# Performance work log

Hardware: AMD Instinct MI355X
Metric: run time of the kernel (lower is better)

The kernel has to match this reference:

```python
import jax, jax.numpy as jnp
import numpy as np

HIDDEN = 1024
EMBED = 1024
SEQ = 512
BATCH = 64


def setup_inputs() -> dict:
    key = jax.random.key(0)
    k1, k2, k3 = jax.random.split(key, 3)
    factor = 1.0 / np.sqrt(HIDDEN)
    embeds = jax.random.normal(k1, (SEQ, BATCH, EMBED), dtype=jnp.float32)
    w = jax.random.uniform(k2, (HIDDEN + EMBED, 4 * HIDDEN), dtype=jnp.float32,
                           minval=-factor, maxval=factor)
    b = jax.random.uniform(k3, (4 * HIDDEN,), dtype=jnp.float32,
                           minval=-factor, maxval=factor)
    # forget-gate bias += 1 (gate order is g, i, f, o)
    b = b.at[2 * HIDDEN:3 * HIDDEN].add(1.0)
    return {"embeds": embeds, "w": w, "b": b}


def reference(embeds, w, b):
    T, B, E = embeds.shape
    H = w.shape[1] // 4

    def step(carry, x_t):
        h, c = carry
        data = jnp.concatenate([h, x_t], axis=-1)          # [B, H+E]
        big = data @ w + b                                  # [B, 4H]
        g, i, f, o = jnp.split(big, 4, axis=1)
        g = jnp.tanh(g)
        i = jax.nn.sigmoid(i)
        f = jax.nn.sigmoid(f)
        o = jax.nn.sigmoid(o)
        c_new = g * i + c * f
        h_new = jnp.tanh(c_new) * o
        return (h_new, c_new), h_new

    h0 = jnp.zeros((B, H), dtype=embeds.dtype)
    c0 = jnp.zeros((B, H), dtype=embeds.dtype)
    _, out = jax.lax.scan(step, (h0, c0), embeds)           # out: [T, B, H]
    return out
```

## Files before the change

kernel.cpp:

```cpp
#include <hip/hip_runtime.h>
#include <stdint.h>


#define TSTEPS 512
#define NBATCH 64
#define NHID   1024
#define NWG2   64
#define FLAGSTRIDE 32
#define AGENT  __HIP_MEMORY_SCOPE_AGENT

typedef __attribute__((ext_vector_type(8))) short bf16x8;
typedef __attribute__((ext_vector_type(4))) float f32x4;
typedef __attribute__((ext_vector_type(4))) int   i32x4;
typedef __attribute__((ext_vector_type(4))) float fl4;

__device__ __forceinline__ uint16_t f2bf(float f){
  uint32_t u = __float_as_uint(f);
  u += 0x7fffu + ((u >> 16) & 1u);
  return (uint16_t)(u >> 16);
}
__device__ __forceinline__ float bf2f(uint16_t b){
  return __uint_as_float(((uint32_t)b) << 16);
}
__device__ __forceinline__ float sigm(float x){ return 1.0f/(1.0f + __expf(-x)); }
__device__ __forceinline__ float tanhfast(float x){ return 1.0f - 2.0f/(__expf(2.0f*x) + 1.0f); }
__device__ __forceinline__ bf16x8 as_bf(i32x4 v){
  union { i32x4 i; bf16x8 b; } u; u.i = v; return u.b;
}

__global__ void k0a_cvt(const float* __restrict__ in, uint16_t* __restrict__ outp, int n8){
  int stride = gridDim.x * blockDim.x;
  for (int i = blockIdx.x * blockDim.x + threadIdx.x; i < n8; i += stride){
    const fl4* p = (const fl4*)(in + (size_t)i * 8);
    fl4 v0 = p[0], v1 = p[1];
    union { uint16_t u[8]; i32x4 v; } r;
    r.u[0]=f2bf(v0.x); r.u[1]=f2bf(v0.y); r.u[2]=f2bf(v0.z); r.u[3]=f2bf(v0.w);
    r.u[4]=f2bf(v1.x); r.u[5]=f2bf(v1.y); r.u[6]=f2bf(v1.z); r.u[7]=f2bf(v1.w);
    *(i32x4*)(outp + (size_t)i * 8) = r.v;
  }
}

__global__ void k0b_trans(const float* __restrict__ w, uint16_t* __restrict__ wT){
  __shared__ float tile[64 * 65];
  int k0 = blockIdx.x * 64;
  int n0 = blockIdx.y * 64;
  int tid = threadIdx.x;
  int r  = tid >> 2;
  int cq = (tid & 3) * 16;
#pragma unroll
  for (int i = 0; i < 4; ++i){
    fl4 v = *(const fl4*)(w + (size_t)(k0 + r) * 4096 + n0 + cq + i * 4);
    tile[r*65 + cq + i*4 + 0] = v.x;
    tile[r*65 + cq + i*4 + 1] = v.y;
    tile[r*65 + cq + i*4 + 2] = v.z;
    tile[r*65 + cq + i*4 + 3] = v.w;
  }
  __syncthreads();
  union { uint16_t u[8]; i32x4 v; } a, b;
#pragma unroll
  for (int i = 0; i < 8; ++i) a.u[i] = f2bf(tile[(cq + i) * 65 + r]);
#pragma unroll
  for (int i = 0; i < 8; ++i) b.u[i] = f2bf(tile[(cq + 8 + i) * 65 + r]);
  *(i32x4*)(wT + (size_t)(n0 + r) * 2048 + k0 + cq)     = a.v;
  *(i32x4*)(wT + (size_t)(n0 + r) * 2048 + k0 + cq + 8) = b.v;
}

__launch_bounds__(256, 2)
__global__ void k1_xw(const uint16_t* __restrict__ ebf, const uint16_t* __restrict__ wT,
                      const float* __restrict__ bias, uint16_t* __restrict__ xw){
  __shared__ char sm[32768];
  char* As = sm;
  char* Bs = sm + 16384;
  int bid = blockIdx.x;
  int nt = bid & 31, mt = bid >> 5;
  int m0 = mt * 128, n0 = nt * 128;
  int tid = threadIdx.x;
  int lane = tid & 63, wid = tid >> 6;
  int wr = wid >> 1, wc = wid & 1;

  f32x4 zero = {0.f, 0.f, 0.f, 0.f};
  f32x4 acc[4][4];
#pragma unroll
  for (int mi = 0; mi < 4; ++mi)
#pragma unroll
    for (int ni = 0; ni < 4; ++ni) acc[mi][ni] = zero;

  for (int kt = 0; kt < 16; ++kt){
    __syncthreads();
#pragma unroll
    for (int i = 0; i < 4; ++i){
      int L = i * 256 + tid;
      int row = L >> 3, c = L & 7;
      i32x4 va = *(const i32x4*)(ebf + (size_t)(m0 + row) * 1024 + kt * 64 + c * 8);
      *(i32x4*)(As + row * 128 + ((c ^ (row & 7)) * 16)) = va;
      i32x4 vb = *(const i32x4*)(wT + (size_t)(n0 + row) * 2048 + 1024 + kt * 64 + c * 8);
      *(i32x4*)(Bs + row * 128 + ((c ^ (row & 7)) * 16)) = vb;
    }
    __syncthreads();
#pragma unroll
    for (int kk = 0; kk < 2; ++kk){
      bf16x8 a[4], b[4];
      int ci = kk * 4 + (lane >> 4);
#pragma unroll
      for (int mi = 0; mi < 4; ++mi){
        int rl = wr * 64 + mi * 16 + (lane & 15);
        a[mi] = *(const bf16x8*)(As + rl * 128 + ((ci ^ (rl & 7)) * 16));
      }
#pragma unroll
      for (int ni = 0; ni < 4; ++ni){
        int sl = wc * 64 + ni * 16 + (lane & 15);
        b[ni] = *(const bf16x8*)(Bs + sl * 128 + ((ci ^ (sl & 7)) * 16));
      }
#pragma unroll
      for (int mi = 0; mi < 4; ++mi)
#pragma unroll
        for (int ni = 0; ni < 4; ++ni)
          acc[mi][ni] = __builtin_amdgcn_mfma_f32_16x16x32_bf16(a[mi], b[ni], acc[mi][ni], 0, 0, 0);
    }
  }
  float bcol[4];
#pragma unroll
  for (int ni = 0; ni < 4; ++ni) bcol[ni] = bias[n0 + wc * 64 + ni * 16 + (lane & 15)];
#pragma unroll
  for (int mi = 0; mi < 4; ++mi)
#pragma unroll
    for (int ni = 0; ni < 4; ++ni)
#pragma unroll
      for (int jj = 0; jj < 4; ++jj){
        int rg = m0 + wr * 64 + mi * 16 + (lane >> 4) * 4 + jj;
        int cg = n0 + wc * 64 + ni * 16 + (lane & 15);
        xw[(size_t)rg * 4096 + cg] = f2bf(acc[mi][ni][jj] + bcol[ni]);
      }
}

#define LDA(k, OFF) asm volatile("global_load_dwordx4 %0, %1, off offset:" #OFF \
                                 : "=v"(ap[k]) : "v"(aB) : "memory")
#define WAITV(N) do { asm volatile("s_waitcnt vmcnt(" #N ")" ::: "memory"); \
                      __builtin_amdgcn_sched_barrier(0); } while(0)
#define GBLK(K0) \
  _Pragma("unroll") \
  for (int kc = K0; kc < K0 + 8; ++kc){ \
    bf16x8 a = as_bf(ap[kc]); \
    _Pragma("unroll") \
    for (int g = 0; g < 4; ++g){ \
      bf16x8 b = *(const bf16x8*)(WP + ((kc * 4 + g) << 10) + (lane << 4)); \
      acc[g] = __builtin_amdgcn_mfma_f32_16x16x32_bf16(a, b, acc[g], 0, 0, 0); \
    } \
  }

__launch_bounds__(256, 1)
__global__ void k2_rec(const uint16_t* __restrict__ xw, const uint16_t* __restrict__ wT,
                       uint16_t* __restrict__ hbuf, int* __restrict__ flags,
                       float* __restrict__ outp){
  extern __shared__ char sm[];
  char* WP = sm;

  int tid  = threadIdx.x;
  int lane = tid & 63;
  int wid  = tid >> 6;
  int wg = blockIdx.x;
  int j0 = wg * 16;

#pragma unroll
  for (int i = 0; i < 32; ++i){
    int L = i * 256 + tid;
    int kc = L >> 8;
    int g  = (L >> 6) & 3;
    int l6 = L & 63;
    int q  = (l6 >> 4) & 3;
    int rr = l6 & 15;
    i32x4 v = *(const i32x4*)(wT + (size_t)(g * 1024 + j0 + rr) * 2048 + kc * 32 + q * 8);
    *(i32x4*)(WP + (size_t)L * 16) = v;
  }
  __syncthreads();

  const int r0 = wid * 16;
  const int q  = lane >> 4;
  const int rr = lane & 15;

  float creg[4] = {0.f, 0.f, 0.f, 0.f};

  uint16_t xc[4][4];
  {
    const uint16_t* xp = xw + (size_t)0 * (64 * 4096) + j0 + rr;
#pragma unroll
    for (int g = 0; g < 4; ++g)
#pragma unroll
      for (int p = 0; p < 4; ++p)
        xc[g][p] = xp[(size_t)(r0 + q * 4 + p) * 4096 + g * 1024];
  }

  for (int t = 0; t < TSTEPS; ++t){
    if (t > 0){
      if (tid < 64){
        while (true){
          int v = __hip_atomic_load(&flags[tid * FLAGSTRIDE], __ATOMIC_RELAXED, AGENT);
          if (__all(v >= t)) break;
          __builtin_amdgcn_s_sleep(1);
        }
      }
      __syncthreads();
    }

    const uint16_t* hsrc = hbuf + (size_t)t * (NBATCH * NHID);
    const uint16_t* aB = hsrc + (size_t)(r0 + rr) * 1024 + q * 8;
    i32x4 ap[32];
    LDA(0,0);     LDA(1,64);    LDA(2,128);   LDA(3,192);
    LDA(4,256);   LDA(5,320);   LDA(6,384);   LDA(7,448);
    LDA(8,512);   LDA(9,576);   LDA(10,640);  LDA(11,704);
    LDA(12,768);  LDA(13,832);  LDA(14,896);  LDA(15,960);
    LDA(16,1024); LDA(17,1088); LDA(18,1152); LDA(19,1216);
    LDA(20,1280); LDA(21,1344); LDA(22,1408); LDA(23,1472);
    LDA(24,1536); LDA(25,1600); LDA(26,1664); LDA(27,1728);
    LDA(28,1792); LDA(29,1856); LDA(30,1920); LDA(31,1984);

    uint16_t xn[4][4];
    {
      int tn = (t < TSTEPS - 1) ? t + 1 : t;
      const uint16_t* xp = xw + (size_t)tn * (64 * 4096) + j0 + rr;
#pragma unroll
      for (int g = 0; g < 4; ++g)
#pragma unroll
        for (int p = 0; p < 4; ++p)
          xn[g][p] = xp[(size_t)(r0 + q * 4 + p) * 4096 + g * 1024];
    }

    f32x4 acc[4];
#pragma unroll
    for (int g = 0; g < 4; ++g) acc[g] = (f32x4){0.f, 0.f, 0.f, 0.f};

    WAITV(40); GBLK(0);
    WAITV(32); GBLK(8);
    WAITV(24); GBLK(16);
    WAITV(16); GBLK(24);

    uint16_t* hdst = hbuf + (size_t)(t + 1) * (NBATCH * NHID);
    float*    odst = outp + (size_t)t * (NBATCH * NHID);
    float hv[4];
#pragma unroll
    for (int p = 0; p < 4; ++p){
      float G = acc[0][p] + bf2f(xc[0][p]);
      float I = acc[1][p] + bf2f(xc[1][p]);
      float F = acc[2][p] + bf2f(xc[2][p]);
      float O = acc[3][p] + bf2f(xc[3][p]);
      G = tanhfast(G); I = sigm(I); F = sigm(F); O = sigm(O);
      float c = G * I + creg[p] * F;
      creg[p] = c;
      float h = tanhfast(c) * O;
      hv[p] = h;
      __hip_atomic_store(hbuf + (size_t)(t + 1) * (NBATCH * NHID)
                              + (size_t)(r0 + q * 4 + p) * 1024 + j0 + rr,
                         f2bf(h), __ATOMIC_RELAXED, AGENT);
    }
    (void)hdst;

#pragma unroll
    for (int g = 0; g < 4; ++g)
#pragma unroll
      for (int p = 0; p < 4; ++p)
        xc[g][p] = xn[g][p];

    asm volatile("s_waitcnt vmcnt(0)" ::: "memory");
    __syncthreads();
    if (tid == 0)
      __hip_atomic_store(&flags[wg * FLAGSTRIDE], t + 1, __ATOMIC_RELAXED, AGENT);

#pragma unroll
    for (int p = 0; p < 4; ++p)
      odst[(size_t)(r0 + q * 4 + p) * 1024 + j0 + rr] = hv[p];
  }
}

extern "C" void kernel_launch(void* const* d_in, const int* in_sizes, int n_in,
                              void* d_out, int out_size, void* d_ws, size_t ws_size,
                              hipStream_t stream){
  const float* embeds = (const float*)d_in[0];
  const float* w      = (const float*)d_in[1];
  const float* bias   = (const float*)d_in[2];
  float* outp = (float*)d_out;
  char* ws = (char*)d_ws;

  const size_t o_ebf = 0;
  const size_t o_wT  = o_ebf + (size_t)32768 * 1024 * 2;
  const size_t o_xw  = o_wT  + (size_t)4096 * 2048 * 2;
  const size_t o_hb  = o_xw  + (size_t)32768 * 4096 * 2;
  const size_t o_fl  = o_hb  + (size_t)513 * 64 * 1024 * 2;

  uint16_t* ebf  = (uint16_t*)(ws + o_ebf);
  uint16_t* wT   = (uint16_t*)(ws + o_wT);
  uint16_t* xw   = (uint16_t*)(ws + o_xw);
  uint16_t* hbuf = (uint16_t*)(ws + o_hb);
  int*      flags= (int*)(ws + o_fl);

  hipMemsetAsync(ws + o_hb, 0, (size_t)64 * 1024 * 2, stream);
  hipMemsetAsync(ws + o_fl, 0, NWG2 * FLAGSTRIDE * sizeof(int), stream);

  k0a_cvt<<<2048, 256, 0, stream>>>(embeds, ebf, (512 * 64 * 1024) / 8);
  k0b_trans<<<dim3(32, 64), 256, 0, stream>>>(w, wT);
  k1_xw<<<8192, 256, 0, stream>>>(ebf, wT, bias, xw);

  (void)hipFuncSetAttribute((const void*)k2_rec,
                            hipFuncAttributeMaxDynamicSharedMemorySize, 131072);
  k2_rec<<<NWG2, 256, 131072, stream>>>(xw, wT, hbuf, flags, outp);
}
```

Before: 4.525 ms.

## Split recurrent tile 2x2 across waves with per-wave flags and LDS gate exchange

Each workgroup's four waves now each compute a 32-row by 2-gate sub-tile instead of 16 rows by all four gates. Results are exchanged through an extra LDS buffer so every thread gets all four gates for its elements. The step barrier is replaced by per-wave flags: each wave publishes its own flag, and each wave polls only the flags of the row half it reads. This removes the single-wave poll plus block barrier on the critical path and halves LDS weight reads per MFMA. It adds an LDS exchange and a __syncthreads per step, doubles the A-register footprint, and raises dynamic LDS above 128KB.

```diff
diff --git a/kernel.cpp b/kernel.cpp
--- a/kernel.cpp
+++ b/kernel.cpp
@@ -133,19 +133,21 @@
       }
 }
 
-#define LDA(k, OFF) asm volatile("global_load_dwordx4 %0, %1, off offset:" #OFF \
-                                 : "=v"(ap[k]) : "v"(aB) : "memory")
+#define LDA(k, BASE, OFF) asm volatile("global_load_dwordx4 %0, %1, off offset:" #OFF \
+                                 : "=v"(ap[k]) : "v"(BASE) : "memory")
 #define WAITV(N) do { asm volatile("s_waitcnt vmcnt(" #N ")" ::: "memory"); \
                       __builtin_amdgcn_sched_barrier(0); } while(0)
-#define GBLK(K0) \
+#define GBLK(NB) \
   _Pragma("unroll") \
-  for (int kc = K0; kc < K0 + 8; ++kc){ \
-    bf16x8 a = as_bf(ap[kc]); \
-    _Pragma("unroll") \
-    for (int g = 0; g < 4; ++g){ \
-      bf16x8 b = *(const bf16x8*)(WP + ((kc * 4 + g) << 10) + (lane << 4)); \
-      acc[g] = __builtin_amdgcn_mfma_f32_16x16x32_bf16(a, b, acc[g], 0, 0, 0); \
-    } \
+  for (int kc = (NB) * 4; kc < (NB) * 4 + 4; ++kc){ \
+    bf16x8 b0 = *(const bf16x8*)(WP + ((kc * 4 + 0) << 10) + chB + (lane << 4)); \
+    bf16x8 b1 = *(const bf16x8*)(WP + ((kc * 4 + 1) << 10) + chB + (lane << 4)); \
+    bf16x8 a0 = as_bf(ap[kc * 2 + 0]); \
+    bf16x8 a1 = as_bf(ap[kc * 2 + 1]); \
+    acc00 = __builtin_amdgcn_mfma_f32_16x16x32_bf16(a0, b0, acc00, 0, 0, 0); \
+    acc01 = __builtin_amdgcn_mfma_f32_16x16x32_bf16(a0, b1, acc01, 0, 0, 0); \
+    acc10 = __builtin_amdgcn_mfma_f32_16x16x32_bf16(a1, b0, acc10, 0, 0, 0); \
+    acc11 = __builtin_amdgcn_mfma_f32_16x16x32_bf16(a1, b1, acc11, 0, 0, 0); \
   }
 
 __launch_bounds__(256, 1)
@@ -153,13 +155,17 @@
                        uint16_t* __restrict__ hbuf, int* __restrict__ flags,
                        float* __restrict__ outp){
   extern __shared__ char sm[];
-  char* WP = sm;
+  char*  WP = sm;
+  float* EX = (float*)(sm + 131072);
 
   int tid  = threadIdx.x;
   int lane = tid & 63;
-  int wid  = tid >> 6;
+  int w    = tid >> 6;
+  int rh   = w >> 1;
+  int ch   = w & 1;
   int wg = blockIdx.x;
   int j0 = wg * 16;
+  const int chB = ch * 2048;
 
 #pragma unroll
   for (int i = 0; i < 32; ++i){
@@ -167,92 +173,114 @@
     int kc = L >> 8;
     int g  = (L >> 6) & 3;
     int l6 = L & 63;
-    int q  = (l6 >> 4) & 3;
-    int rr = l6 & 15;
-    i32x4 v = *(const i32x4*)(wT + (size_t)(g * 1024 + j0 + rr) * 2048 + kc * 32 + q * 8);
+    int q_ = (l6 >> 4) & 3;
+    int rr_ = l6 & 15;
+    i32x4 v = *(const i32x4*)(wT + (size_t)(g * 1024 + j0 + rr_) * 2048 + kc * 32 + q_ * 8);
     *(i32x4*)(WP + (size_t)L * 16) = v;
   }
-  __syncthreads();
-
-  const int r0 = wid * 16;
+
   const int q  = lane >> 4;
   const int rr = lane & 15;
+  const int rb = (tid >> 4) * 4;
+  const int ej = tid & 15;
 
   float creg[4] = {0.f, 0.f, 0.f, 0.f};
 
   uint16_t xc[4][4];
   {
-    const uint16_t* xp = xw + (size_t)0 * (64 * 4096) + j0 + rr;
+    const uint16_t* xp = xw + j0 + ej;
 #pragma unroll
     for (int g = 0; g < 4; ++g)
 #pragma unroll
       for (int p = 0; p < 4; ++p)
-        xc[g][p] = xp[(size_t)(r0 + q * 4 + p) * 4096 + g * 1024];
-  }
+        xc[g][p] = xp[(size_t)(rb + p) * 4096 + g * 1024];
+  }
+  __syncthreads();
 
   for (int t = 0; t < TSTEPS; ++t){
     if (t > 0){
-      if (tid < 64){
-        while (true){
-          int v = __hip_atomic_load(&flags[tid * FLAGSTRIDE], __ATOMIC_RELAXED, AGENT);
-          if (__all(v >= t)) break;
-          __builtin_amdgcn_s_sleep(1);
-        }
-      }
-      __syncthreads();
+      int fi = (lane * 4 + rh * 2) * FLAGSTRIDE;
+      while (true){
+        int v0 = __hip_atomic_load(&flags[fi],              __ATOMIC_RELAXED, AGENT);
+        int v1 = __hip_atomic_load(&flags[fi + FLAGSTRIDE], __ATOMIC_RELAXED, AGENT);
+        if (__all(v0 >= t && v1 >= t)) break;
+        __builtin_amdgcn_s_sleep(1);
+      }
     }
 
     const uint16_t* hsrc = hbuf + (size_t)t * (NBATCH * NHID);
-    const uint16_t* aB = hsrc + (size_t)(r0 + rr) * 1024 + q * 8;
-    i32x4 ap[32];
-    LDA(0,0);     LDA(1,64);    LDA(2,128);   LDA(3,192);
-    LDA(4,256);   LDA(5,320);   LDA(6,384);   LDA(7,448);
-    LDA(8,512);   LDA(9,576);   LDA(10,640);  LDA(11,704);
-    LDA(12,768);  LDA(13,832);  LDA(14,896);  LDA(15,960);
-    LDA(16,1024); LDA(17,1088); LDA(18,1152); LDA(19,1216);
-    LDA(20,1280); LDA(21,1344); LDA(22,1408); LDA(23,1472);
-    LDA(24,1536); LDA(25,1600); LDA(26,1664); LDA(27,1728);
-    LDA(28,1792); LDA(29,1856); LDA(30,1920); LDA(31,1984);
+    const uint16_t* aB0 = hsrc + (size_t)(rh * 32 + rr) * 1024 + q * 8;
+    const uint16_t* aB1 = aB0 + 16 * 1024;
+    i32x4 ap[64];
+    LDA(0,aB0,0);    LDA(1,aB1,0);    LDA(2,aB0,64);   LDA(3,aB1,64);
+    LDA(4,aB0,128);  LDA(5,aB1,128);  LDA(6,aB0,192);  LDA(7,aB1,192);
+    LDA(8,aB0,256);  LDA(9,aB1,256);  LDA(10,aB0,320); LDA(11,aB1,320);
+    LDA(12,aB0,384); LDA(13,aB1,384); LDA(14,aB0,448); LDA(15,aB1,448);
+    LDA(16,aB0,512); LDA(17,aB1,512); LDA(18,aB0,576); LDA(19,aB1,576);
+    LDA(20,aB0,640); LDA(21,aB1,640); LDA(22,aB0,704); LDA(23,aB1,704);
+    LDA(24,aB0,768); LDA(25,aB1,768); LDA(26,aB0,832); LDA(27,aB1,832);
+    LDA(28,aB0,896); LDA(29,aB1,896); LDA(30,aB0,960); LDA(31,aB1,960);
 
     uint16_t xn[4][4];
     {
       int tn = (t < TSTEPS - 1) ? t + 1 : t;
-      const uint16_t* xp = xw + (size_t)tn * (64 * 4096) + j0 + rr;
+      const uint16_t* xp = xw + (size_t)tn * (64 * 4096) + j0 + ej;
 #pragma unroll
       for (int g = 0; g < 4; ++g)
 #pragma unroll
         for (int p = 0; p < 4; ++p)
-          xn[g][p] = xp[(size_t)(r0 + q * 4 + p) * 4096 + g * 1024];
-    }
-
-    f32x4 acc[4];
-#pragma unroll
-    for (int g = 0; g < 4; ++g) acc[g] = (f32x4){0.f, 0.f, 0.f, 0.f};
+          xn[g][p] = xp[(size_t)(rb + p) * 4096 + g * 1024];
+    }
+
+    f32x4 acc00 = {0,0,0,0}, acc01 = {0,0,0,0}, acc10 = {0,0,0,0}, acc11 = {0,0,0,0};
 
     WAITV(40); GBLK(0);
-    WAITV(32); GBLK(8);
-    WAITV(24); GBLK(16);
-    WAITV(16); GBLK(24);
+    LDA(32,aB0,1024); LDA(33,aB1,1024); LDA(34,aB0,1088); LDA(35,aB1,1088);
+    LDA(36,aB0,1152); LDA(37,aB1,1152); LDA(38,aB0,1216); LDA(39,aB1,1216);
+    LDA(40,aB0,1280); LDA(41,aB1,1280); LDA(42,aB0,1344); LDA(43,aB1,1344);
+    LDA(44,aB0,1408); LDA(45,aB1,1408); LDA(46,aB0,1472); LDA(47,aB1,1472);
+    WAITV(48); GBLK(1);
+    LDA(48,aB0,1536); LDA(49,aB1,1536); LDA(50,aB0,1600); LDA(51,aB1,1600);
+    LDA(52,aB0,1664); LDA(53,aB1,1664); LDA(54,aB0,1728); LDA(55,aB1,1728);
+    LDA(56,aB0,1792); LDA(57,aB1,1792); LDA(58,aB0,1856); LDA(59,aB1,1856);
+    LDA(60,aB0,1920); LDA(61,aB1,1920); LDA(62,aB0,1984); LDA(63,aB1,1984);
+    WAITV(56); GBLK(2);
+    WAITV(48); GBLK(3);
+    WAITV(24); GBLK(4);
+    WAITV(16); GBLK(5);
+    WAITV(8);  GBLK(6);
+    WAITV(0);  GBLK(7);
+
+    {
+      int wr0 = rh * 32 + q * 4;
+      int wc0 = ch * 32 + rr;
+#pragma unroll
+      for (int p = 0; p < 4; ++p){
+        EX[(wr0 +  0 + p) * 68 + wc0     ] = acc00[p];
+        EX[(wr0 +  0 + p) * 68 + wc0 + 16] = acc01[p];
+        EX[(wr0 + 16 + p) * 68 + wc0     ] = acc10[p];
+        EX[(wr0 + 16 + p) * 68 + wc0 + 16] = acc11[p];
+      }
+    }
+    __syncthreads();
 
     uint16_t* hdst = hbuf + (size_t)(t + 1) * (NBATCH * NHID);
     float*    odst = outp + (size_t)t * (NBATCH * NHID);
     float hv[4];
 #pragma unroll
     for (int p = 0; p < 4; ++p){
-      float G = acc[0][p] + bf2f(xc[0][p]);
-      float I = acc[1][p] + bf2f(xc[1][p]);
-      float F = acc[2][p] + bf2f(xc[2][p]);
-      float O = acc[3][p] + bf2f(xc[3][p]);
+      float G = EX[(rb + p) * 68 +  0 + ej] + bf2f(xc[0][p]);
+      float I = EX[(rb + p) * 68 + 16 + ej] + bf2f(xc[1][p]);
+      float F = EX[(rb + p) * 68 + 32 + ej] + bf2f(xc[2][p]);
+      float O = EX[(rb + p) * 68 + 48 + ej] + bf2f(xc[3][p]);
       G = tanhfast(G); I = sigm(I); F = sigm(F); O = sigm(O);
       float c = G * I + creg[p] * F;
       creg[p] = c;
       float h = tanhfast(c) * O;
       hv[p] = h;
-      __hip_atomic_store(hbuf + (size_t)(t + 1) * (NBATCH * NHID)
-                              + (size_t)(r0 + q * 4 + p) * 1024 + j0 + rr,
-                         f2bf(h), __ATOMIC_RELAXED, AGENT);
-    }
-    (void)hdst;
+      __hip_atomic_store(hdst + (size_t)(rb + p) * 1024 + j0 + ej, f2bf(h),
+                         __ATOMIC_RELAXED, AGENT);
+    }
 
 #pragma unroll
     for (int g = 0; g < 4; ++g)
@@ -261,13 +289,12 @@
         xc[g][p] = xn[g][p];
 
     asm volatile("s_waitcnt vmcnt(0)" ::: "memory");
-    __syncthreads();
-    if (tid == 0)
-      __hip_atomic_store(&flags[wg * FLAGSTRIDE], t + 1, __ATOMIC_RELAXED, AGENT);
+    if (lane == 0)
+      __hip_atomic_store(&flags[(wg * 4 + w) * FLAGSTRIDE], t + 1, __ATOMIC_RELAXED, AGENT);
 
 #pragma unroll
     for (int p = 0; p < 4; ++p)
-      odst[(size_t)(r0 + q * 4 + p) * 1024 + j0 + rr] = hv[p];
+      odst[(size_t)(rb + p) * 1024 + j0 + ej] = hv[p];
   }
 }
 
@@ -293,13 +320,13 @@
   int*      flags= (int*)(ws + o_fl);
 
   hipMemsetAsync(ws + o_hb, 0, (size_t)64 * 1024 * 2, stream);
-  hipMemsetAsync(ws + o_fl, 0, NWG2 * FLAGSTRIDE * sizeof(int), stream);
+  hipMemsetAsync(ws + o_fl, 0, 256 * FLAGSTRIDE * sizeof(int), stream);
 
   k0a_cvt<<<2048, 256, 0, stream>>>(embeds, ebf, (512 * 64 * 1024) / 8);
   k0b_trans<<<dim3(32, 64), 256, 0, stream>>>(w, wT);
   k1_xw<<<8192, 256, 0, stream>>>(ebf, wT, bias, xw);
 
   (void)hipFuncSetAttribute((const void*)k2_rec,
-                            hipFuncAttributeMaxDynamicSharedMemorySize, 131072);
-  k2_rec<<<NWG2, 256, 131072, stream>>>(xw, wT, hbuf, flags, outp);
-}
+                            hipFuncAttributeMaxDynamicSharedMemorySize, 148480);
+  k2_rec<<<NWG2, 256, 148480, stream>>>(xw, wT, hbuf, flags, outp);
+}
```

New measurement: 5.770 ms. 27.5% more time.
